# Kernel optimization log

Measured on AMD Instinct MI355X. Metric: run time of the kernel, lower is better.

## Reference

```python
import jax, jax.numpy as jnp
import numpy as np

N = 65536      # occupied voxels
C = 64         # in/out channels
H = 4          # heads
D = 16         # attn channels per head
KVOL = 125     # kernel_size^3 for kernel_size=5, dim=3
P = 1048576    # sparse neighbor pairs (~16 per voxel)


def _l2norm(t):
    # torch F.normalize(p=2, dim=-1): x / max(||x||, 1e-12)
    n = jnp.linalg.norm(t, axis=-1, keepdims=True)
    return t / jnp.maximum(n, 1e-12)


def setup_inputs() -> dict:
    key = jax.random.key(0)
    ks = jax.random.split(key, 10)
    s = 1.0 / np.sqrt(C)
    x = jax.random.normal(ks[0], (N, C), dtype=jnp.float32)
    Wq = jax.random.normal(ks[1], (C, C), dtype=jnp.float32) * s
    Wk = jax.random.normal(ks[2], (C, C), dtype=jnp.float32) * s
    Wv = jax.random.normal(ks[3], (C, C), dtype=jnp.float32) * s
    Wo = jax.random.normal(ks[4], (C, C), dtype=jnp.float32) * s
    bq = jnp.zeros((C,), jnp.float32)
    bk = jnp.zeros((C,), jnp.float32)
    bv = jnp.zeros((C,), jnp.float32)
    bo = jnp.zeros((C,), jnp.float32)
    pos_enc = jax.random.normal(ks[5], (KVOL, H, D), dtype=jnp.float32)  # inter_pos_enc ~ N(0,1)
    in_idx = jax.random.randint(ks[6], (P,), 0, N)
    kern_idx = jax.random.randint(ks[7], (P,), 0, KVOL)
    out_idx = jax.random.randint(ks[8], (P,), 0, N)
    kq_map = jnp.stack([in_idx * KVOL + kern_idx, out_idx]).astype(jnp.int32)
    return dict(x=x, Wq=Wq, bq=bq, Wk=Wk, bk=bk, Wv=Wv, bv=bv, Wo=Wo, bo=bo,
                pos_enc=pos_enc, kq_map=kq_map)


def reference(x, Wq, bq, Wk, bk, Wv, bv, Wo, bo, pos_enc, kq_map):
    q = (x @ Wq + bq).reshape(N, H, D)
    k = (x @ Wk + bk).reshape(N, H, D)
    v = (x @ Wv + bv).reshape(N, H, D)
    nq = _l2norm(q)
    nk = _l2norm(k)
    npos = _l2norm(pos_enc)
    in_idx = kq_map[0] // KVOL   # key voxel index
    kidx = kq_map[0] % KVOL      # kernel offset index
    out_idx = kq_map[1]          # query voxel index
    # per-pair attention weight (cosine attention + relative pos-enc, no softmax)
    attn = jnp.einsum('phd,phd->ph', nq[out_idx], nk[in_idx] + npos[kidx])
    # scatter weighted values to query voxels
    msg = attn[:, :, None] * v[in_idx]                     # [P,H,D]
    out = jax.ops.segment_sum(msg, out_idx, num_segments=N)  # [N,H,D]
    out = out.reshape(N, C) @ Wo + bo
    return out + x  # residual add (SparseTensor + stensor)
```

## Files before the change

### kernel.cpp

```cpp
#include <hip/hip_runtime.h>
#include <hip/hip_fp16.h>

#define NVOX 65536
#define KVOL 125
#define NPAIR 1048576
#define CAP 48
#define QKV_BLOCKS 768
#define FILL_BLOCKS 2048
#define MERGED_BLOCKS (QKV_BLOCKS + FILL_BLOCKS)
#define GATH_BLOCKS 1024

typedef _Float16 half8 __attribute__((ext_vector_type(8)));
typedef float f32x4 __attribute__((ext_vector_type(4)));

__global__ __launch_bounds__(256) void zero_cursor_kernel(int4* __restrict__ c4)
{
    c4[blockIdx.x * 256 + threadIdx.x] = make_int4(0, 0, 0, 0);
}

__global__ __launch_bounds__(256, 3) void qkv_fill_kernel(
    const float* __restrict__ x,
    const float* __restrict__ Wq, const float* __restrict__ bq,
    const float* __restrict__ Wk, const float* __restrict__ bk,
    const float* __restrict__ Wv, const float* __restrict__ bv,
    __half* __restrict__ nqh, signed char* __restrict__ ktab,
    __half* __restrict__ vtab,
    const float* __restrict__ pos, const int* __restrict__ kq_map,
    __half* __restrict__ nposh, int* __restrict__ cursor,
    unsigned int* __restrict__ pairlist)
{
    __shared__ _Float16 wth[3 * 64 * 72];
    const int tid  = threadIdx.x;
    const int lane = tid & 63;
    const int wid  = tid >> 6;
    const int grp  = blockIdx.x / 11;
    const int sub  = blockIdx.x - grp * 11;

    if (sub >= 3) {
        const int fb = grp * 8 + (sub - 3);
        if (fb < KVOL && wid == 0) {
            const float pv = pos[fb * 64 + lane];
            float s = pv * pv;
            #pragma unroll
            for (int m = 1; m <= 8; m <<= 1) s += __shfl_xor(s, m);
            nposh[fb * 64 + lane] = __float2half(pv / fmaxf(sqrtf(s), 1e-12f));
        }
        const int gtid = fb * 256 + tid;
        const int p0 = gtid;
        const int p1 = gtid + 524288;
        const unsigned k0 = (unsigned)kq_map[p0];
        const unsigned k1 = (unsigned)kq_map[p1];
        const int o0 = kq_map[NPAIR + p0];
        const int o1 = kq_map[NPAIR + p1];
        const int r0 = atomicAdd(&cursor[o0], 1);
        const int r1 = atomicAdd(&cursor[o1], 1);
        const unsigned i0 = k0 / 125u, i1 = k1 / 125u;
        if (r0 < CAP) pairlist[(size_t)o0 * CAP + ((r0 & 3) * 12 + (r0 >> 2))]
                        = (i0 << 7) | (k0 - i0 * 125u);
        if (r1 < CAP) pairlist[(size_t)o1 * CAP + ((r1 & 3) * 12 + (r1 >> 2))]
                        = (i1 << 7) | (k1 - i1 * 125u);
        return;
    }

    const int qb = grp * 3 + sub;
    for (int idx = tid; idx < 3 * 4096; idx += 256) {
        const int m = idx >> 12;
        const int r = idx & 4095;
        const int k = r >> 6;
        const int c = r & 63;
        const float wv = (m == 0 ? Wq : (m == 1 ? Wk : Wv))[k * 64 + c];
        wth[(m * 64 + c) * 72 + k] = (_Float16)wv;
    }
    __syncthreads();

    const int lr = lane & 15;
    const int kg = lane >> 4;
    const int gw = qb * 4 + wid;

    for (int tile = gw; tile < 4096; tile += 3072) {
        const int nb = tile << 4;
        half8 af[2];
        #pragma unroll
        for (int ks = 0; ks < 2; ++ks) {
            const float4 xa = *(const float4*)&x[(size_t)(nb + lr) * 64 + ks * 32 + kg * 8];
            const float4 xb = *(const float4*)&x[(size_t)(nb + lr) * 64 + ks * 32 + kg * 8 + 4];
            half8 t;
            t[0] = (_Float16)xa.x; t[1] = (_Float16)xa.y;
            t[2] = (_Float16)xa.z; t[3] = (_Float16)xa.w;
            t[4] = (_Float16)xb.x; t[5] = (_Float16)xb.y;
            t[6] = (_Float16)xb.z; t[7] = (_Float16)xb.w;
            af[ks] = t;
        }
        #pragma unroll
        for (int m = 0; m < 3; ++m) {
            const float* bp = (m == 0 ? bq : (m == 1 ? bk : bv));
            #pragma unroll
            for (int t = 0; t < 4; ++t) {
                f32x4 c = {0.f, 0.f, 0.f, 0.f};
                #pragma unroll
                for (int ks = 0; ks < 2; ++ks) {
                    const half8 bf = *(const half8*)&wth[(m * 64 + t * 16 + lr) * 72 + ks * 32 + kg * 8];
                    c = __builtin_amdgcn_mfma_f32_16x16x32_f16(af[ks], bf, c, 0, 0, 0);
                }
                const float bias = bp[t * 16 + lr];
                if (m < 2) {
                    #pragma unroll
                    for (int r = 0; r < 4; ++r) {
                        const float av = c[r] + bias;
                        float s = av * av;
                        s += __shfl_xor(s, 1); s += __shfl_xor(s, 2);
                        s += __shfl_xor(s, 4); s += __shfl_xor(s, 8);
                        const float inv = av / fmaxf(sqrtf(s), 1e-12f);
                        const size_t o = (size_t)(nb + kg * 4 + r) * 64 + t * 16 + lr;
                        if (m == 0) nqh[o] = __float2half(inv);
                        else        ktab[o] = (signed char)__float2int_rn(inv * 127.f);
                    }
                } else {
                    #pragma unroll
                    for (int r = 0; r < 4; ++r) {
                        const size_t o = (size_t)(nb + kg * 4 + r) * 64 + t * 16 + lr;
                        vtab[o] = __float2half(c[r] + bias);
                    }
                }
            }
        }
    }
}

__device__ __forceinline__ void pair_accum(
    unsigned pk, unsigned kk, uint2 vv, const __half* npos_s, int cc,
    const float4& a4, const float4& a4s, float4& ac)
{
    const int kidx = (int)(pk & 127u);
    const __half2* np = (const __half2*)&npos_s[kidx * 64 + cc];
    const float2 c01 = __half22float2(np[0]);
    const float2 c23 = __half22float2(np[1]);
    const int ki = (int)kk;
    const float k0 = (float)(signed char)(ki);
    const float k1 = (float)(signed char)(ki >> 8);
    const float k2 = (float)(signed char)(ki >> 16);
    const float k3 = (float)(ki >> 24);
    float pdot = a4s.x * k0 + a4s.y * k1 + a4s.z * k2 + a4s.w * k3
               + a4.x * c01.x + a4.y * c01.y + a4.z * c23.x + a4.w * c23.y;
    pdot += __shfl_xor(pdot, 1);
    pdot += __shfl_xor(pdot, 2);
    const float2 v01 = __half22float2(*(const __half2*)&vv.x);
    const float2 v23 = __half22float2(*(const __half2*)&vv.y);
    ac.x += pdot * v01.x; ac.y += pdot * v01.y;
    ac.z += pdot * v23.x; ac.w += pdot * v23.y;
}

__device__ __forceinline__ void quad_accum(
    uint4 u, const signed char* __restrict__ ktab, const __half* __restrict__ vtab,
    const __half* npos_s, int cc, const float4& a4, const float4& a4s, float4& ac)
{
    const unsigned kk0 = *(const unsigned*)(ktab + (size_t)(u.x >> 7) * 64 + cc);
    const unsigned kk1 = *(const unsigned*)(ktab + (size_t)(u.y >> 7) * 64 + cc);
    const unsigned kk2 = *(const unsigned*)(ktab + (size_t)(u.z >> 7) * 64 + cc);
    const unsigned kk3 = *(const unsigned*)(ktab + (size_t)(u.w >> 7) * 64 + cc);
    const uint2 vv0 = *(const uint2*)(vtab + (size_t)(u.x >> 7) * 64 + cc);
    const uint2 vv1 = *(const uint2*)(vtab + (size_t)(u.y >> 7) * 64 + cc);
    const uint2 vv2 = *(const uint2*)(vtab + (size_t)(u.z >> 7) * 64 + cc);
    const uint2 vv3 = *(const uint2*)(vtab + (size_t)(u.w >> 7) * 64 + cc);
    pair_accum(u.x, kk0, vv0, npos_s, cc, a4, a4s, ac);
    pair_accum(u.y, kk1, vv1, npos_s, cc, a4, a4s, ac);
    pair_accum(u.z, kk2, vv2, npos_s, cc, a4, a4s, ac);
    pair_accum(u.w, kk3, vv3, npos_s, cc, a4, a4s, ac);
}

__device__ __forceinline__ void tail_accum(
    uint4 u, int r, const signed char* __restrict__ ktab, const __half* __restrict__ vtab,
    const __half* npos_s, int cc, const float4& a4, const float4& a4s, float4& ac)
{
    if (r > 0) {
        const unsigned kk = *(const unsigned*)(ktab + (size_t)(u.x >> 7) * 64 + cc);
        const uint2 vv = *(const uint2*)(vtab + (size_t)(u.x >> 7) * 64 + cc);
        pair_accum(u.x, kk, vv, npos_s, cc, a4, a4s, ac);
    }
    if (r > 1) {
        const unsigned kk = *(const unsigned*)(ktab + (size_t)(u.y >> 7) * 64 + cc);
        const uint2 vv = *(const uint2*)(vtab + (size_t)(u.y >> 7) * 64 + cc);
        pair_accum(u.y, kk, vv, npos_s, cc, a4, a4s, ac);
    }
    if (r > 2) {
        const unsigned kk = *(const unsigned*)(ktab + (size_t)(u.z >> 7) * 64 + cc);
        const uint2 vv = *(const uint2*)(vtab + (size_t)(u.z >> 7) * 64 + cc);
        pair_accum(u.z, kk, vv, npos_s, cc, a4, a4s, ac);
    }
}

__global__ __launch_bounds__(256, 4) void gather_out_kernel(
    const int* __restrict__ cursor, const unsigned int* __restrict__ pairlist,
    const __half* __restrict__ nqh, const signed char* __restrict__ ktab,
    const __half* __restrict__ vtab, const __half* __restrict__ nposh,
    const float* __restrict__ Wo, const float* __restrict__ bo,
    const float* __restrict__ x, float* __restrict__ out)
{
    __shared__ float wo_s[4096];
    __shared__ __half npos_s[8192];
    __shared__ float ms[4][4][64];
    const int tid = threadIdx.x;
    for (int i = tid; i < 1024; i += 256) ((float4*)wo_s)[i] = ((const float4*)Wo)[i];
    for (int i = tid; i < 1000; i += 256) ((uint4*)npos_s)[i] = ((const uint4*)nposh)[i];
    __syncthreads();

    const int lane = tid & 63;
    const int wid  = tid >> 6;
    const int l    = lane & 15;
    const int pg   = lane >> 4;
    const int cc   = l * 4;
    const int gw   = blockIdx.x * 4 + wid;
    const float4 bo4 = *(const float4*)&bo[cc];

    for (int nb = gw * 4; nb < NVOX; nb += GATH_BLOCKS * 16) {
        #pragma unroll
        for (int v = 0; v < 4; ++v) {
            const int n = nb + v;
            const uint2 qp = *(const uint2*)(nqh + (size_t)n * 64 + cc);
            const float2 q01 = __half22float2(*(const __half2*)&qp.x);
            const float2 q23 = __half22float2(*(const __half2*)&qp.y);
            const float4 a4 = make_float4(q01.x, q01.y, q23.x, q23.y);
            const float4 a4s = make_float4(a4.x * (1.f / 127.f), a4.y * (1.f / 127.f),
                                           a4.z * (1.f / 127.f), a4.w * (1.f / 127.f));
            const int cnt = min(cursor[n], CAP);
            const int m = (cnt > pg) ? ((cnt - pg + 3) >> 2) : 0;
            const uint4* pb = (const uint4*)(pairlist + (size_t)n * CAP + pg * 12);
            const uint4 u0 = pb[0];
            const uint4 u1 = pb[1];
            const uint4 u2 = pb[2];
            float4 acc = make_float4(0.f, 0.f, 0.f, 0.f);
            int rem = m;
            if (rem >= 4) { quad_accum(u0, ktab, vtab, npos_s, cc, a4, a4s, acc); rem -= 4; }
            else          { tail_accum(u0, rem, ktab, vtab, npos_s, cc, a4, a4s, acc); rem = 0; }
            if (rem >= 4) { quad_accum(u1, ktab, vtab, npos_s, cc, a4, a4s, acc); rem -= 4; }
            else if (rem > 0) { tail_accum(u1, rem, ktab, vtab, npos_s, cc, a4, a4s, acc); rem = 0; }
            if (rem >= 4) { quad_accum(u2, ktab, vtab, npos_s, cc, a4, a4s, acc); rem -= 4; }
            else if (rem > 0) { tail_accum(u2, rem, ktab, vtab, npos_s, cc, a4, a4s, acc); rem = 0; }
            acc.x += __shfl_xor(acc.x, 16); acc.y += __shfl_xor(acc.y, 16);
            acc.z += __shfl_xor(acc.z, 16); acc.w += __shfl_xor(acc.w, 16);
            acc.x += __shfl_xor(acc.x, 32); acc.y += __shfl_xor(acc.y, 32);
            acc.z += __shfl_xor(acc.z, 32); acc.w += __shfl_xor(acc.w, 32);
            if (pg == 0) *(float4*)&ms[wid][v][cc] = acc;
        }
        __syncthreads();
        float4 o4[4];
        #pragma unroll
        for (int v = 0; v < 4; ++v) o4[v] = make_float4(0.f, 0.f, 0.f, 0.f);
        #pragma unroll
        for (int ib = 0; ib < 4; ++ib) {
            float4 mq[4];
            #pragma unroll
            for (int v = 0; v < 4; ++v)
                mq[v] = *(const float4*)&ms[wid][v][pg * 16 + ib * 4];
            #pragma unroll
            for (int tt = 0; tt < 4; ++tt) {
                const int j = pg * 16 + ib * 4 + tt;
                const float4 w4 = *(const float4*)&wo_s[j * 64 + cc];
                #pragma unroll
                for (int v = 0; v < 4; ++v) {
                    const float m = (tt == 0 ? mq[v].x : tt == 1 ? mq[v].y :
                                     tt == 2 ? mq[v].z : mq[v].w);
                    o4[v].x += m * w4.x; o4[v].y += m * w4.y;
                    o4[v].z += m * w4.z; o4[v].w += m * w4.w;
                }
            }
        }
        #pragma unroll
        for (int v = 0; v < 4; ++v) {
            o4[v].x += __shfl_xor(o4[v].x, 16); o4[v].y += __shfl_xor(o4[v].y, 16);
            o4[v].z += __shfl_xor(o4[v].z, 16); o4[v].w += __shfl_xor(o4[v].w, 16);
            o4[v].x += __shfl_xor(o4[v].x, 32); o4[v].y += __shfl_xor(o4[v].y, 32);
            o4[v].z += __shfl_xor(o4[v].z, 32); o4[v].w += __shfl_xor(o4[v].w, 32);
        }
        if (pg == 0) {
            #pragma unroll
            for (int v = 0; v < 4; ++v) {
                const float4 xr = *(const float4*)&x[(size_t)(nb + v) * 64 + cc];
                float4 r;
                r.x = o4[v].x + bo4.x + xr.x;
                r.y = o4[v].y + bo4.y + xr.y;
                r.z = o4[v].z + bo4.z + xr.z;
                r.w = o4[v].w + bo4.w + xr.w;
                *(float4*)&out[(size_t)(nb + v) * 64 + cc] = r;
            }
        }
        __syncthreads();
    }
}

extern "C" void kernel_launch(void* const* d_in, const int* in_sizes, int n_in,
                              void* d_out, int out_size, void* d_ws, size_t ws_size,
                              hipStream_t stream) {
    const float* x   = (const float*)d_in[0];
    const float* Wq  = (const float*)d_in[1];
    const float* bq  = (const float*)d_in[2];
    const float* Wk  = (const float*)d_in[3];
    const float* bk  = (const float*)d_in[4];
    const float* Wv  = (const float*)d_in[5];
    const float* bv  = (const float*)d_in[6];
    const float* Wo  = (const float*)d_in[7];
    const float* bo  = (const float*)d_in[8];
    const float* pos = (const float*)d_in[9];
    const int*   kq  = (const int*)d_in[10];

    char* w = (char*)d_ws;
    __half*       nqh      = (__half*)w;       w += (size_t)NVOX * 64 * 2;
    __half*       vtab     = (__half*)w;       w += (size_t)NVOX * 64 * 2;
    signed char*  ktab     = (signed char*)w;  w += (size_t)NVOX * 64;
    unsigned int* pairlist = (unsigned int*)w; w += (size_t)NVOX * CAP * 4;
    int*          cursor   = (int*)w;          w += (size_t)NVOX * 4;
    __half*       nposh    = (__half*)w;       w += 16384;

    zero_cursor_kernel<<<64, 256, 0, stream>>>((int4*)cursor);
    qkv_fill_kernel<<<MERGED_BLOCKS, 256, 0, stream>>>(x, Wq, bq, Wk, bk, Wv, bv,
                                                       nqh, ktab, vtab,
                                                       pos, kq, nposh, cursor, pairlist);
    gather_out_kernel<<<GATH_BLOCKS, 256, 0, stream>>>(cursor, pairlist, nqh, ktab, vtab,
                                                       nposh, Wo, bo, x, (float*)d_out);
}
```

Baseline: 222.7 us.

## Fuse zero, QKV/fill and gather stages into one cooperative kernel with grid syncs

Replaces the three separate launches (cursor zeroing, QKV projection plus pair-list fill, gather/output) with a single cooperative kernel of 1024 blocks that uses grid-wide syncs between phases. Each block now does one QKV tile per wave and fills four pairs per thread, and the shared-memory buffers are reused across phases. The aim is to remove launch gaps and tail effects between kernels. In exchange the grid is fixed at 1024 blocks, grid barriers add cost, the QKV phase loses occupancy-driven overlap with the fill phase, and the old three-kernel path is kept as a fallback if the cooperative launch fails.

```diff
diff --git a/kernel.cpp b/kernel.cpp
--- a/kernel.cpp
+++ b/kernel.cpp
@@ -1,10 +1,14 @@
 #include <hip/hip_runtime.h>
 #include <hip/hip_fp16.h>
+#include <hip/hip_cooperative_groups.h>
+
+namespace cg = cooperative_groups;
 
 #define NVOX 65536
 #define KVOL 125
 #define NPAIR 1048576
 #define CAP 48
+#define FUSED_BLOCKS 1024
 #define QKV_BLOCKS 768
 #define FILL_BLOCKS 2048
 #define MERGED_BLOCKS (QKV_BLOCKS + FILL_BLOCKS)
@@ -13,56 +17,77 @@
 typedef _Float16 half8 __attribute__((ext_vector_type(8)));
 typedef float f32x4 __attribute__((ext_vector_type(4)));
 
-__global__ __launch_bounds__(256) void zero_cursor_kernel(int4* __restrict__ c4)
-{
-    c4[blockIdx.x * 256 + threadIdx.x] = make_int4(0, 0, 0, 0);
-}
-
-__global__ __launch_bounds__(256, 3) void qkv_fill_kernel(
+__device__ __forceinline__ void pair_accum(
+    unsigned pk, unsigned kk, uint2 vv, const __half* npos_s, int cc,
+    const float4& a4, const float4& a4s, float4& ac)
+{
+    const int kidx = (int)(pk & 127u);
+    const __half2* np = (const __half2*)&npos_s[kidx * 64 + cc];
+    const float2 c01 = __half22float2(np[0]);
+    const float2 c23 = __half22float2(np[1]);
+    const int ki = (int)kk;
+    const float k0 = (float)(signed char)(ki);
+    const float k1 = (float)(signed char)(ki >> 8);
+    const float k2 = (float)(signed char)(ki >> 16);
+    const float k3 = (float)(ki >> 24);
+    float pdot = a4s.x * k0 + a4s.y * k1 + a4s.z * k2 + a4s.w * k3
+               + a4.x * c01.x + a4.y * c01.y + a4.z * c23.x + a4.w * c23.y;
+    pdot += __shfl_xor(pdot, 1);
+    pdot += __shfl_xor(pdot, 2);
+    const float2 v01 = __half22float2(*(const __half2*)&vv.x);
+    const float2 v23 = __half22float2(*(const __half2*)&vv.y);
+    ac.x += pdot * v01.x; ac.y += pdot * v01.y;
+    ac.z += pdot * v23.x; ac.w += pdot * v23.y;
+}
+
+__device__ __forceinline__ void quad_accum(
+    uint4 u, const signed char* __restrict__ ktab, const __half* __restrict__ vtab,
+    const __half* npos_s, int cc, const float4& a4, const float4& a4s, float4& ac)
+{
+    const unsigned kk0 = *(const unsigned*)(ktab + (size_t)(u.x >> 7) * 64 + cc);
+    const unsigned kk1 = *(const unsigned*)(ktab + (size_t)(u.y >> 7) * 64 + cc);
+    const unsigned kk2 = *(const unsigned*)(ktab + (size_t)(u.z >> 7) * 64 + cc);
+    const unsigned kk3 = *(const unsigned*)(ktab + (size_t)(u.w >> 7) * 64 + cc);
+    const uint2 vv0 = *(const uint2*)(vtab + (size_t)(u.x >> 7) * 64 + cc);
+    const uint2 vv1 = *(const uint2*)(vtab + (size_t)(u.y >> 7) * 64 + cc);
+    const uint2 vv2 = *(const uint2*)(vtab + (size_t)(u.z >> 7) * 64 + cc);
+    const uint2 vv3 = *(const uint2*)(vtab + (size_t)(u.w >> 7) * 64 + cc);
+    pair_accum(u.x, kk0, vv0, npos_s, cc, a4, a4s, ac);
+    pair_accum(u.y, kk1, vv1, npos_s, cc, a4, a4s, ac);
+    pair_accum(u.z, kk2, vv2, npos_s, cc, a4, a4s, ac);
+    pair_accum(u.w, kk3, vv3, npos_s, cc, a4, a4s, ac);
+}
+
+__device__ __forceinline__ void tail_accum(
+    uint4 u, int r, const signed char* __restrict__ ktab, const __half* __restrict__ vtab,
+    const __half* npos_s, int cc, const float4& a4, const float4& a4s, float4& ac)
+{
+    if (r > 0) {
+        const unsigned kk = *(const unsigned*)(ktab + (size_t)(u.x >> 7) * 64 + cc);
+        const uint2 vv = *(const uint2*)(vtab + (size_t)(u.x >> 7) * 64 + cc);
+        pair_accum(u.x, kk, vv, npos_s, cc, a4, a4s, ac);
+    }
+    if (r > 1) {
+        const unsigned kk = *(const unsigned*)(ktab + (size_t)(u.y >> 7) * 64 + cc);
+        const uint2 vv = *(const uint2*)(vtab + (size_t)(u.y >> 7) * 64 + cc);
+        pair_accum(u.y, kk, vv, npos_s, cc, a4, a4s, ac);
+    }
+    if (r > 2) {
+        const unsigned kk = *(const unsigned*)(ktab + (size_t)(u.z >> 7) * 64 + cc);
+        const uint2 vv = *(const uint2*)(vtab + (size_t)(u.z >> 7) * 64 + cc);
+        pair_accum(u.z, kk, vv, npos_s, cc, a4, a4s, ac);
+    }
+}
+
+__device__ __forceinline__ void qkv_body(
+    _Float16* wth, int tid, int lane, int nb_base_wave,
     const float* __restrict__ x,
     const float* __restrict__ Wq, const float* __restrict__ bq,
     const float* __restrict__ Wk, const float* __restrict__ bk,
     const float* __restrict__ Wv, const float* __restrict__ bv,
     __half* __restrict__ nqh, signed char* __restrict__ ktab,
-    __half* __restrict__ vtab,
-    const float* __restrict__ pos, const int* __restrict__ kq_map,
-    __half* __restrict__ nposh, int* __restrict__ cursor,
-    unsigned int* __restrict__ pairlist)
-{
-    __shared__ _Float16 wth[3 * 64 * 72];
-    const int tid  = threadIdx.x;
-    const int lane = tid & 63;
-    const int wid  = tid >> 6;
-    const int grp  = blockIdx.x / 11;
-    const int sub  = blockIdx.x - grp * 11;
-
-    if (sub >= 3) {
-        const int fb = grp * 8 + (sub - 3);
-        if (fb < KVOL && wid == 0) {
-            const float pv = pos[fb * 64 + lane];
-            float s = pv * pv;
-            #pragma unroll
-            for (int m = 1; m <= 8; m <<= 1) s += __shfl_xor(s, m);
-            nposh[fb * 64 + lane] = __float2half(pv / fmaxf(sqrtf(s), 1e-12f));
-        }
-        const int gtid = fb * 256 + tid;
-        const int p0 = gtid;
-        const int p1 = gtid + 524288;
-        const unsigned k0 = (unsigned)kq_map[p0];
-        const unsigned k1 = (unsigned)kq_map[p1];
-        const int o0 = kq_map[NPAIR + p0];
-        const int o1 = kq_map[NPAIR + p1];
-        const int r0 = atomicAdd(&cursor[o0], 1);
-        const int r1 = atomicAdd(&cursor[o1], 1);
-        const unsigned i0 = k0 / 125u, i1 = k1 / 125u;
-        if (r0 < CAP) pairlist[(size_t)o0 * CAP + ((r0 & 3) * 12 + (r0 >> 2))]
-                        = (i0 << 7) | (k0 - i0 * 125u);
-        if (r1 < CAP) pairlist[(size_t)o1 * CAP + ((r1 & 3) * 12 + (r1 >> 2))]
-                        = (i1 << 7) | (k1 - i1 * 125u);
-        return;
-    }
-
-    const int qb = grp * 3 + sub;
+    __half* __restrict__ vtab, int tiles_stride, int do_loop)
+{
     for (int idx = tid; idx < 3 * 4096; idx += 256) {
         const int m = idx >> 12;
         const int r = idx & 4095;
@@ -75,9 +100,8 @@
 
     const int lr = lane & 15;
     const int kg = lane >> 4;
-    const int gw = qb * 4 + wid;
-
-    for (int tile = gw; tile < 4096; tile += 3072) {
+
+    for (int tile = nb_base_wave; tile < 4096; tile += tiles_stride) {
         const int nb = tile << 4;
         half8 af[2];
         #pragma unroll
@@ -124,82 +148,18 @@
                 }
             }
         }
-    }
-}
-
-__device__ __forceinline__ void pair_accum(
-    unsigned pk, unsigned kk, uint2 vv, const __half* npos_s, int cc,
-    const float4& a4, const float4& a4s, float4& ac)
-{
-    const int kidx = (int)(pk & 127u);
-    const __half2* np = (const __half2*)&npos_s[kidx * 64 + cc];
-    const float2 c01 = __half22float2(np[0]);
-    const float2 c23 = __half22float2(np[1]);
-    const int ki = (int)kk;
-    const float k0 = (float)(signed char)(ki);
-    const float k1 = (float)(signed char)(ki >> 8);
-    const float k2 = (float)(signed char)(ki >> 16);
-    const float k3 = (float)(ki >> 24);
-    float pdot = a4s.x * k0 + a4s.y * k1 + a4s.z * k2 + a4s.w * k3
-               + a4.x * c01.x + a4.y * c01.y + a4.z * c23.x + a4.w * c23.y;
-    pdot += __shfl_xor(pdot, 1);
-    pdot += __shfl_xor(pdot, 2);
-    const float2 v01 = __half22float2(*(const __half2*)&vv.x);
-    const float2 v23 = __half22float2(*(const __half2*)&vv.y);
-    ac.x += pdot * v01.x; ac.y += pdot * v01.y;
-    ac.z += pdot * v23.x; ac.w += pdot * v23.y;
-}
-
-__device__ __forceinline__ void quad_accum(
-    uint4 u, const signed char* __restrict__ ktab, const __half* __restrict__ vtab,
-    const __half* npos_s, int cc, const float4& a4, const float4& a4s, float4& ac)
-{
-    const unsigned kk0 = *(const unsigned*)(ktab + (size_t)(u.x >> 7) * 64 + cc);
-    const unsigned kk1 = *(const unsigned*)(ktab + (size_t)(u.y >> 7) * 64 + cc);
-    const unsigned kk2 = *(const unsigned*)(ktab + (size_t)(u.z >> 7) * 64 + cc);
-    const unsigned kk3 = *(const unsigned*)(ktab + (size_t)(u.w >> 7) * 64 + cc);
-    const uint2 vv0 = *(const uint2*)(vtab + (size_t)(u.x >> 7) * 64 + cc);
-    const uint2 vv1 = *(const uint2*)(vtab + (size_t)(u.y >> 7) * 64 + cc);
-    const uint2 vv2 = *(const uint2*)(vtab + (size_t)(u.z >> 7) * 64 + cc);
-    const uint2 vv3 = *(const uint2*)(vtab + (size_t)(u.w >> 7) * 64 + cc);
-    pair_accum(u.x, kk0, vv0, npos_s, cc, a4, a4s, ac);
-    pair_accum(u.y, kk1, vv1, npos_s, cc, a4, a4s, ac);
-    pair_accum(u.z, kk2, vv2, npos_s, cc, a4, a4s, ac);
-    pair_accum(u.w, kk3, vv3, npos_s, cc, a4, a4s, ac);
-}
-
-__device__ __forceinline__ void tail_accum(
-    uint4 u, int r, const signed char* __restrict__ ktab, const __half* __restrict__ vtab,
-    const __half* npos_s, int cc, const float4& a4, const float4& a4s, float4& ac)
-{
-    if (r > 0) {
-        const unsigned kk = *(const unsigned*)(ktab + (size_t)(u.x >> 7) * 64 + cc);
-        const uint2 vv = *(const uint2*)(vtab + (size_t)(u.x >> 7) * 64 + cc);
-        pair_accum(u.x, kk, vv, npos_s, cc, a4, a4s, ac);
-    }
-    if (r > 1) {
-        const unsigned kk = *(const unsigned*)(ktab + (size_t)(u.y >> 7) * 64 + cc);
-        const uint2 vv = *(const uint2*)(vtab + (size_t)(u.y >> 7) * 64 + cc);
-        pair_accum(u.y, kk, vv, npos_s, cc, a4, a4s, ac);
-    }
-    if (r > 2) {
-        const unsigned kk = *(const unsigned*)(ktab + (size_t)(u.z >> 7) * 64 + cc);
-        const uint2 vv = *(const uint2*)(vtab + (size_t)(u.z >> 7) * 64 + cc);
-        pair_accum(u.z, kk, vv, npos_s, cc, a4, a4s, ac);
-    }
-}
-
-__global__ __launch_bounds__(256, 4) void gather_out_kernel(
+        if (!do_loop) break;
+    }
+}
+
+__device__ __forceinline__ void gather_body(
+    float* wo_s, __half* npos_s, float* ms, int tid,
     const int* __restrict__ cursor, const unsigned int* __restrict__ pairlist,
     const __half* __restrict__ nqh, const signed char* __restrict__ ktab,
     const __half* __restrict__ vtab, const __half* __restrict__ nposh,
     const float* __restrict__ Wo, const float* __restrict__ bo,
-    const float* __restrict__ x, float* __restrict__ out)
-{
-    __shared__ float wo_s[4096];
-    __shared__ __half npos_s[8192];
-    __shared__ float ms[4][4][64];
-    const int tid = threadIdx.x;
+    const float* __restrict__ x, float* __restrict__ out, int bid)
+{
     for (int i = tid; i < 1024; i += 256) ((float4*)wo_s)[i] = ((const float4*)Wo)[i];
     for (int i = tid; i < 1000; i += 256) ((uint4*)npos_s)[i] = ((const uint4*)nposh)[i];
     __syncthreads();
@@ -209,7 +169,7 @@
     const int l    = lane & 15;
     const int pg   = lane >> 4;
     const int cc   = l * 4;
-    const int gw   = blockIdx.x * 4 + wid;
+    const int gw   = bid * 4 + wid;
     const float4 bo4 = *(const float4*)&bo[cc];
 
     for (int nb = gw * 4; nb < NVOX; nb += GATH_BLOCKS * 16) {
@@ -240,7 +200,7 @@
             acc.z += __shfl_xor(acc.z, 16); acc.w += __shfl_xor(acc.w, 16);
             acc.x += __shfl_xor(acc.x, 32); acc.y += __shfl_xor(acc.y, 32);
             acc.z += __shfl_xor(acc.z, 32); acc.w += __shfl_xor(acc.w, 32);
-            if (pg == 0) *(float4*)&ms[wid][v][cc] = acc;
+            if (pg == 0) *(float4*)&ms[(wid * 4 + v) * 64 + cc] = acc;
         }
         __syncthreads();
         float4 o4[4];
@@ -251,7 +211,7 @@
             float4 mq[4];
             #pragma unroll
             for (int v = 0; v < 4; ++v)
-                mq[v] = *(const float4*)&ms[wid][v][pg * 16 + ib * 4];
+                mq[v] = *(const float4*)&ms[(wid * 4 + v) * 64 + pg * 16 + ib * 4];
             #pragma unroll
             for (int tt = 0; tt < 4; ++tt) {
                 const int j = pg * 16 + ib * 4 + tt;
@@ -286,6 +246,139 @@
         }
         __syncthreads();
     }
+}
+
+__global__ __launch_bounds__(256, 4) void fused_kernel(
+    const float* __restrict__ x,
+    const float* __restrict__ Wq, const float* __restrict__ bq,
+    const float* __restrict__ Wk, const float* __restrict__ bk,
+    const float* __restrict__ Wv, const float* __restrict__ bv,
+    const float* __restrict__ Wo, const float* __restrict__ bo,
+    const float* __restrict__ pos, const int* __restrict__ kq_map,
+    __half* __restrict__ nqh, signed char* __restrict__ ktab,
+    __half* __restrict__ vtab, __half* __restrict__ nposh,
+    int* __restrict__ cursor, unsigned int* __restrict__ pairlist,
+    float* __restrict__ out)
+{
+    __shared__ __align__(16) char smem[36864];
+    const int tid  = threadIdx.x;
+    const int bid  = blockIdx.x;
+    const int lane = tid & 63;
+    const int wid  = tid >> 6;
+    cg::grid_group grid = cg::this_grid();
+
+    {
+        const int zi = bid * 256 + tid;
+        if (zi < NVOX / 4) ((int4*)cursor)[zi] = make_int4(0, 0, 0, 0);
+    }
+    __threadfence();
+    grid.sync();
+    __threadfence();
+
+    {
+        _Float16* wth = (_Float16*)smem;
+        if (bid < KVOL && wid == 0) {
+            const float pv = pos[bid * 64 + lane];
+            float s = pv * pv;
+            #pragma unroll
+            for (int m = 1; m <= 8; m <<= 1) s += __shfl_xor(s, m);
+            nposh[bid * 64 + lane] = __float2half(pv / fmaxf(sqrtf(s), 1e-12f));
+        }
+        qkv_body(wth, tid, lane, bid * 4 + wid, x, Wq, bq, Wk, bk, Wv, bv,
+                 nqh, ktab, vtab, 4096, 0);
+    }
+
+    {
+        const int gt = bid * 256 + tid;
+        #pragma unroll
+        for (int kq4 = 0; kq4 < 4; ++kq4) {
+            const int p = gt + kq4 * 262144;
+            const unsigned kk = (unsigned)kq_map[p];
+            const int oo = kq_map[NPAIR + p];
+            const int r = atomicAdd(&cursor[oo], 1);
+            const unsigned ii = kk / 125u;
+            if (r < CAP) pairlist[(size_t)oo * CAP + ((r & 3) * 12 + (r >> 2))]
+                            = (ii << 7) | (kk - ii * 125u);
+        }
+    }
+    __threadfence();
+    grid.sync();
+    __threadfence();
+
+    {
+        float*  wo_s   = (float*)smem;
+        __half* npos_s = (__half*)(smem + 16384);
+        float*  ms     = (float*)(smem + 32768);
+        gather_body(wo_s, npos_s, ms, tid, cursor, pairlist, nqh, ktab, vtab,
+                    nposh, Wo, bo, x, out, bid);
+    }
+}
+
+__global__ __launch_bounds__(256) void zero_cursor_kernel(int4* __restrict__ c4)
+{
+    c4[blockIdx.x * 256 + threadIdx.x] = make_int4(0, 0, 0, 0);
+}
+
+__global__ __launch_bounds__(256, 3) void qkv_fill_kernel(
+    const float* __restrict__ x,
+    const float* __restrict__ Wq, const float* __restrict__ bq,
+    const float* __restrict__ Wk, const float* __restrict__ bk,
+    const float* __restrict__ Wv, const float* __restrict__ bv,
+    __half* __restrict__ nqh, signed char* __restrict__ ktab,
+    __half* __restrict__ vtab,
+    const float* __restrict__ pos, const int* __restrict__ kq_map,
+    __half* __restrict__ nposh, int* __restrict__ cursor,
+    unsigned int* __restrict__ pairlist)
+{
+    __shared__ _Float16 wth[3 * 64 * 72];
+    const int tid  = threadIdx.x;
+    const int lane = tid & 63;
+    const int wid  = tid >> 6;
+    const int grp  = blockIdx.x / 11;
+    const int sub  = blockIdx.x - grp * 11;
+
+    if (sub >= 3) {
+        const int fb = grp * 8 + (sub - 3);
+        if (fb < KVOL && wid == 0) {
+            const float pv = pos[fb * 64 + lane];
+            float s = pv * pv;
+            #pragma unroll
+            for (int m = 1; m <= 8; m <<= 1) s += __shfl_xor(s, m);
+            nposh[fb * 64 + lane] = __float2half(pv / fmaxf(sqrtf(s), 1e-12f));
+        }
+        const int gtid = fb * 256 + tid;
+        const int p0 = gtid;
+        const int p1 = gtid + 524288;
+        const unsigned k0 = (unsigned)kq_map[p0];
+        const unsigned k1 = (unsigned)kq_map[p1];
+        const int o0 = kq_map[NPAIR + p0];
+        const int o1 = kq_map[NPAIR + p1];
+        const int r0 = atomicAdd(&cursor[o0], 1);
+        const int r1 = atomicAdd(&cursor[o1], 1);
+        const unsigned i0 = k0 / 125u, i1 = k1 / 125u;
+        if (r0 < CAP) pairlist[(size_t)o0 * CAP + ((r0 & 3) * 12 + (r0 >> 2))]
+                        = (i0 << 7) | (k0 - i0 * 125u);
+        if (r1 < CAP) pairlist[(size_t)o1 * CAP + ((r1 & 3) * 12 + (r1 >> 2))]
+                        = (i1 << 7) | (k1 - i1 * 125u);
+        return;
+    }
+
+    const int qb = grp * 3 + sub;
+    qkv_body(wth, tid, lane, qb * 4 + wid, x, Wq, bq, Wk, bk, Wv, bv,
+             nqh, ktab, vtab, 3072, 1);
+}
+
+__global__ __launch_bounds__(256, 4) void gather_out_kernel(
+    const int* __restrict__ cursor, const unsigned int* __restrict__ pairlist,
+    const __half* __restrict__ nqh, const signed char* __restrict__ ktab,
+    const __half* __restrict__ vtab, const __half* __restrict__ nposh,
+    const float* __restrict__ Wo, const float* __restrict__ bo,
+    const float* __restrict__ x, float* __restrict__ out)
+{
+    __shared__ __align__(16) char smem[36864];
+    gather_body((float*)smem, (__half*)(smem + 16384), (float*)(smem + 32768),
+                threadIdx.x, cursor, pairlist, nqh, ktab, vtab, nposh,
+                Wo, bo, x, out, blockIdx.x);
 }
 
 extern "C" void kernel_launch(void* const* d_in, const int* in_sizes, int n_in,
@@ -310,11 +403,22 @@
     unsigned int* pairlist = (unsigned int*)w; w += (size_t)NVOX * CAP * 4;
     int*          cursor   = (int*)w;          w += (size_t)NVOX * 4;
     __half*       nposh    = (__half*)w;       w += 16384;
-
-    zero_cursor_kernel<<<64, 256, 0, stream>>>((int4*)cursor);
-    qkv_fill_kernel<<<MERGED_BLOCKS, 256, 0, stream>>>(x, Wq, bq, Wk, bk, Wv, bv,
-                                                       nqh, ktab, vtab,
-                                                       pos, kq, nposh, cursor, pairlist);
-    gather_out_kernel<<<GATH_BLOCKS, 256, 0, stream>>>(cursor, pairlist, nqh, ktab, vtab,
-                                                       nposh, Wo, bo, x, (float*)d_out);
-}
+    float*        outp     = (float*)d_out;
+
+    void* args[] = { (void*)&x, (void*)&Wq, (void*)&bq, (void*)&Wk, (void*)&bk,
+                     (void*)&Wv, (void*)&bv, (void*)&Wo, (void*)&bo, (void*)&pos,
+                     (void*)&kq, (void*)&nqh, (void*)&ktab, (void*)&vtab,
+                     (void*)&nposh, (void*)&cursor, (void*)&pairlist, (void*)&outp };
+    hipError_t err = hipLaunchCooperativeKernel((const void*)fused_kernel,
+                                                dim3(FUSED_BLOCKS), dim3(256),
+                                                args, 0, stream);
+    if (err != hipSuccess) {
+        (void)hipGetLastError();
+        zero_cursor_kernel<<<64, 256, 0, stream>>>((int4*)cursor);
+        qkv_fill_kernel<<<MERGED_BLOCKS, 256, 0, stream>>>(x, Wq, bq, Wk, bk, Wv, bv,
+                                                           nqh, ktab, vtab,
+                                                           pos, kq, nposh, cursor, pairlist);
+        gather_out_kernel<<<GATH_BLOCKS, 256, 0, stream>>>(cursor, pairlist, nqh, ktab,
+                                                           vtab, nposh, Wo, bo, x, outp);
+    }
+}
```

Result: slower. 682.3 us (+206.3%).
